# Performance work log

Measured on AMD Instinct MI355X. Metric: run time of the kernel, lower is better.

The kernel has to match this reference:

```python
import jax, jax.numpy as jnp
import numpy as np

T = 32            # num_tsteps
B = 8192          # batch_size
W_IN0, W_OUT0 = 36, 18
W_IN1, W_OUT1 = 18, 8
TILE0, TILE1 = 2, 1
BETA = (0.95, 0.95)
TH = (0.55, 0.25)
Q = 15000.0       # sephia mrr_Q
ER_DB = 20.0      # sephia extinction ratio
IL_DB = 0.0       # sephia insertion loss
SHIFT_PM = -250.0 # sephia resonance shift per unit spike
P_UNITY = 1e-4    # dbm_to_watt(-10): optical power per WDM channel at unit input


def _lif(inp, mem, beta, th):
    # snntorch Leaky, reset_mechanism='zero', reset_delay=True:
    # reset decided from incoming mem, membrane zeroed before leak+integrate.
    reset = (mem > th).astype(inp.dtype)
    mem_new = (beta * mem + inp) * (1.0 - reset)
    spk = (mem_new > th).astype(inp.dtype)
    return spk, mem_new


def _allpass(spk, wl_nm):
    # All-pass MRR modulator: spike shifts the ring resonance by SHIFT_PM.
    # Normalized detuning delta = shift / (FWHM/2), FWHM = lambda / Q.
    fwhm_pm = wl_nm * 1e3 / Q                      # [C]
    delta = (spk * SHIFT_PM) / (0.5 * fwhm_pm)     # [B, C]
    gamma = 10.0 ** (-ER_DB / 20.0)                # on-resonance amplitude (ER)
    il = 10.0 ** (-IL_DB / 20.0)                   # insertion loss factor
    return (il * (1j * delta + gamma) / (1j * delta + 1.0)).astype(jnp.complex64)


def setup_inputs() -> dict:
    key = jax.random.key(0)
    ks = jax.random.split(key, 6)
    return {
        "x_in": jax.random.uniform(ks[0], (T, B, W_IN0), jnp.float32),
        "W0": jax.random.uniform(ks[1], (TILE0, W_IN0 // TILE0, W_OUT0 * 2 // TILE0), jnp.float32),
        "d0": jax.random.normal(ks[2], (TILE0, W_OUT0 // TILE0), jnp.float32) * 5e3,
        "W1": jax.random.uniform(ks[3], (TILE1, W_IN1 // TILE1, W_OUT1 * 2 // TILE1), jnp.float32),
        "d1": jax.random.normal(ks[4], (TILE1, W_OUT1 // TILE1), jnp.float32) * 5e3,
        "peak_powers_dbm": jax.random.uniform(ks[5], (W_IN0,), jnp.float32, -15.0, -5.0),
    }


def reference(x_in, W0, d0, W1, d1, peak_powers_dbm):
    wl0 = 1550.0 + 0.8 * jnp.arange(W_OUT0, dtype=jnp.float32)   # MRR resonance wavelengths (nm)
    # sephia_inputs: sqrt(dbm_to_watt(P_dbm) * 1e6) field amplitude per channel
    amp0 = jnp.sqrt((10.0 ** (peak_powers_dbm[:W_OUT0] / 10.0) / 1000.0) * 1e6)
    S0 = W_OUT0 * 2 // TILE0   # 18 spatial channels after EO broadcast
    S1 = W_OUT1 * 2 // TILE1   # 16 spatial channels into layer 1

    def step(carry, x_t):
        mem0, mem1 = carry
        b = x_t.shape[0]
        # --- EO conversion + layer 0 MRR weight bank (power domain) ---
        p_in = x_t * P_UNITY                                     # [B, 36] optical power
        p0 = jnp.broadcast_to(p_in[:, :, None], (b, W_IN0, S0)).reshape(b, TILE0, W_IN0 // TILE0, S0)
        I0 = jnp.einsum('btws,tws->bts', p0, W0)                 # photocurrents [B,2,18]
        cur0 = ((I0[..., 0::2] - I0[..., 1::2]) * d0).reshape(b, W_OUT0)  # balanced PDs + Diagonal
        spk0, mem0 = _lif(cur0, mem0, BETA[0], TH[0])
        # --- SEPhIA all-pass MRR modulation of comb lines ---
        lo = _allpass(spk0, wl0) * amp0.astype(jnp.complex64)    # [B, 18] complex field
        pw0 = jnp.abs(lo) ** 2                                   # detected power == spike record
        # --- post-SEPhIA broadcast + layer 1 weight bank ---
        p1 = jnp.broadcast_to(pw0[:, :, None], (b, W_IN1, S1)).reshape(b, TILE1, W_IN1 // TILE1, S1)
        I1 = jnp.einsum('btws,tws->bts', p1, W1)                 # [B,1,16]
        cur1 = ((I1[..., 0::2] - I1[..., 1::2]) * d1).reshape(b, W_OUT1)
        spk1, mem1 = _lif(cur1, mem1, BETA[1], TH[1])
        return (mem0, mem1), (pw0, spk1, mem0, mem1)

    mem0 = jnp.zeros((x_in.shape[1], W_OUT0), x_in.dtype)
    mem1 = jnp.zeros((x_in.shape[1], W_OUT1), x_in.dtype)
    _, (spks0, spks1, mems0, mems1) = jax.lax.scan(step, (mem0, mem1), x_in)
    return spks0, spks1, mems0, mems1
```

## Files before the change

kernel.cpp:

```cpp
#include <hip/hip_runtime.h>


namespace {
constexpr int Tn = 32;
constexpr int Bn = 8192;
constexpr int O_PW = 0;
constexpr int O_S1 = Tn * Bn * 18;
constexpr int O_M0 = O_S1 + Tn * Bn * 8;
constexpr int O_M1 = O_M0 + Tn * Bn * 18;
}

__global__ __launch_bounds__(256, 4)
void oesnn_kernel(const float* __restrict__ x_in,
                  const float* __restrict__ W0g,
                  const float* __restrict__ d0g,
                  const float* __restrict__ W1g,
                  const float* __restrict__ d1g,
                  const float* __restrict__ peakg,
                  float* __restrict__ out)
{
    const int tid = blockIdx.x * 256 + threadIdx.x;
    const int b   = tid >> 5;
    const int g   = tid & 31;
    const int eb  = threadIdx.x >> 5;
    const bool isL0 = (g < 18);
    const bool isL1 = (g >= 18) && (g < 26);

    __shared__ float pwsh[8][20];

    float wA[18], wB[18];
    float dd = 0.f, pon = 0.f, poff = 0.f;
    int tl = 0;

    if (isL0) {
        tl = g / 9;
        const int jc = g % 9;
        dd = d0g[tl * 9 + jc];
        #pragma unroll
        for (int w = 0; w < 18; ++w) {
            const float2 p = *(const float2*)(W0g + ((tl * 18 + w) * 18 + 2 * jc));
            wA[w] = p.x;
            wB[w] = p.y;
        }
        const int c = g;
        const float wl    = 1550.0f + 0.8f * (float)c;
        const float halfw = 0.5f * (wl * 1e3f / 15000.0f);
        const float amp   = sqrtf((exp10f(peakg[c] / 10.0f) / 1000.0f) * 1e6f);
        {
            const float lr = 0.1f * amp;
            const float a  = sqrtf(lr * lr);
            poff = a * a;
        }
        {
            const float delta = -250.0f / halfw;
            const float den = fmaf(delta, delta, 1.0f);
            const float qr  = fmaf(delta, delta, 0.1f) / den;
            const float qi  = (delta - 0.1f * delta) / den;
            const float lr = qr * amp, li = qi * amp;
            const float a  = sqrtf(fmaf(lr, lr, li * li));
            pon = a * a;
        }
    } else {
        const int o = (g < 26) ? (g - 18) : 7;
        dd = d1g[o];
        #pragma unroll
        for (int w = 0; w < 18; ++w) {
            const float2 p = *(const float2*)(W1g + w * 16 + 2 * o);
            wA[w] = p.x;
            wB[w] = p.y;
        }
    }

    float mem0 = 0.f;
    float mem1 = 0.f;

    const float* xp = x_in + (size_t)b * 36 + tl * 18;
    float* opw = out + O_PW + (size_t)b * 18 + g;
    float* om0 = out + O_M0 + (size_t)b * 18 + g;
    const int o1 = isL1 ? (g - 18) : 0;
    float* os1 = out + O_S1 + (size_t)b * 8 + o1;
    float* om1 = out + O_M1 + (size_t)b * 8 + o1;

    float2 xv[9];
    if (isL0) {
        #pragma unroll
        for (int k = 0; k < 9; ++k) xv[k] = *(const float2*)(xp + 2 * k);
    }

    #pragma unroll 1
    for (int t = 0; t < Tn; ++t) {
        if (isL0) {
            float p[18];
            #pragma unroll
            for (int k = 0; k < 9; ++k) {
                p[2 * k]     = xv[k].x * 1e-4f;
                p[2 * k + 1] = xv[k].y * 1e-4f;
            }
            xp += Bn * 36;
            if (t < Tn - 1) {
                #pragma unroll
                for (int k = 0; k < 9; ++k) xv[k] = *(const float2*)(xp + 2 * k);
            }
            float se = 0.f, so = 0.f;
            #pragma unroll
            for (int w = 0; w < 18; ++w) {
                se = fmaf(p[w], wA[w], se);
                so = fmaf(p[w], wB[w], so);
            }
            const float c0 = (se - so) * dd;
            const float m2 = (mem0 > 0.55f) ? 0.0f : fmaf(0.95f, mem0, c0);
            mem0 = m2;
            const float pw = (m2 > 0.55f) ? pon : poff;

            *opw = pw;
            *om0 = m2;
            pwsh[eb][g] = pw;
        }

        if (isL1) {
            const float4 qa = *(const float4*)&pwsh[eb][0];
            const float4 qb = *(const float4*)&pwsh[eb][4];
            const float4 qc = *(const float4*)&pwsh[eb][8];
            const float4 qd = *(const float4*)&pwsh[eb][12];
            const float2 qe = *(const float2*)&pwsh[eb][16];
            const float pwall[18] = {qa.x, qa.y, qa.z, qa.w,
                                     qb.x, qb.y, qb.z, qb.w,
                                     qc.x, qc.y, qc.z, qc.w,
                                     qd.x, qd.y, qd.z, qd.w,
                                     qe.x, qe.y};
            float i1e = 0.f, i1o = 0.f;
            #pragma unroll
            for (int c = 0; c < 18; ++c) {
                i1e = fmaf(pwall[c], wA[c], i1e);
                i1o = fmaf(pwall[c], wB[c], i1o);
            }
            const float c1 = (i1e - i1o) * dd;
            const float m3 = (mem1 > 0.25f) ? 0.0f : fmaf(0.95f, mem1, c1);
            mem1 = m3;
            *os1 = (m3 > 0.25f) ? 1.0f : 0.0f;
            *om1 = m3;
        }

        opw += Bn * 18;
        om0 += Bn * 18;
        os1 += Bn * 8;
        om1 += Bn * 8;
    }
}

extern "C" void kernel_launch(void* const* d_in, const int* in_sizes, int n_in,
                              void* d_out, int out_size, void* d_ws, size_t ws_size,
                              hipStream_t stream) {
    (void)in_sizes; (void)n_in; (void)out_size; (void)d_ws; (void)ws_size;
    const float* x  = (const float*)d_in[0];
    const float* W0 = (const float*)d_in[1];
    const float* d0 = (const float*)d_in[2];
    const float* W1 = (const float*)d_in[3];
    const float* d1 = (const float*)d_in[4];
    const float* pk = (const float*)d_in[5];
    float* out = (float*)d_out;

    dim3 grid(Bn * 32 / 256), block(256);
    hipLaunchKernelGGL(oesnn_kernel, grid, block, 0, stream,
                       x, W0, d0, W1, d1, pk, out);
}
```

Baseline: 137.9 us.

## Software-pipeline layer1 one step behind layer0 with double-buffered shared spikes

Restructures the time loop to process two timesteps per iteration. Layer-1 work for step t runs interleaved with layer-0 work for step t+1, using double-buffered LDS slots, so that the two layers' latencies can overlap. The x inputs are now prefetched two steps ahead into two register buffers by all lanes, including non-L0 lanes. In exchange, register pressure rises and the idle lanes issue redundant loads. Correctness depends on the 64-wide wavefront executing in lockstep, since there are no barriers between the LDS write and read.

```diff
diff --git a/kernel.cpp b/kernel.cpp
--- a/kernel.cpp
+++ b/kernel.cpp
@@ -22,18 +22,18 @@
     const int tid = blockIdx.x * 256 + threadIdx.x;
     const int b   = tid >> 5;
     const int g   = tid & 31;
-    const int eb  = threadIdx.x >> 5;
+    const int wv  = threadIdx.x >> 6;
+    const int eh  = (threadIdx.x >> 5) & 1;
     const bool isL0 = (g < 18);
     const bool isL1 = (g >= 18) && (g < 26);
 
-    __shared__ float pwsh[8][20];
+    __shared__ float pwsh[4][2][2][20];
 
     float wA[18], wB[18];
     float dd = 0.f, pon = 0.f, poff = 0.f;
-    int tl = 0;
+    const int tl = isL0 ? (g / 9) : 0;
 
     if (isL0) {
-        tl = g / 9;
         const int jc = g % 9;
         dd = d0g[tl * 9 + jc];
         #pragma unroll
@@ -74,55 +74,28 @@
     float mem0 = 0.f;
     float mem1 = 0.f;
 
-    const float* xp = x_in + (size_t)b * 36 + tl * 18;
+    const float* xb = x_in + (size_t)b * 36 + tl * 18;
     float* opw = out + O_PW + (size_t)b * 18 + g;
     float* om0 = out + O_M0 + (size_t)b * 18 + g;
     const int o1 = isL1 ? (g - 18) : 0;
     float* os1 = out + O_S1 + (size_t)b * 8 + o1;
     float* om1 = out + O_M1 + (size_t)b * 8 + o1;
 
-    float2 xv[9];
-    if (isL0) {
+    float2 xvA[9], xvB[9];
+    {
+        const float2* s0 = (const float2*)(xb);
+        const float2* s1 = (const float2*)(xb + (size_t)Bn * 36);
         #pragma unroll
-        for (int k = 0; k < 9; ++k) xv[k] = *(const float2*)(xp + 2 * k);
+        for (int k = 0; k < 9; ++k) { xvA[k] = s0[k]; xvB[k] = s1[k]; }
     }
 
-    #pragma unroll 1
-    for (int t = 0; t < Tn; ++t) {
-        if (isL0) {
-            float p[18];
-            #pragma unroll
-            for (int k = 0; k < 9; ++k) {
-                p[2 * k]     = xv[k].x * 1e-4f;
-                p[2 * k + 1] = xv[k].y * 1e-4f;
-            }
-            xp += Bn * 36;
-            if (t < Tn - 1) {
-                #pragma unroll
-                for (int k = 0; k < 9; ++k) xv[k] = *(const float2*)(xp + 2 * k);
-            }
-            float se = 0.f, so = 0.f;
-            #pragma unroll
-            for (int w = 0; w < 18; ++w) {
-                se = fmaf(p[w], wA[w], se);
-                so = fmaf(p[w], wB[w], so);
-            }
-            const float c0 = (se - so) * dd;
-            const float m2 = (mem0 > 0.55f) ? 0.0f : fmaf(0.95f, mem0, c0);
-            mem0 = m2;
-            const float pw = (m2 > 0.55f) ? pon : poff;
-
-            *opw = pw;
-            *om0 = m2;
-            pwsh[eb][g] = pw;
-        }
-
+    auto l1phase = [&](int parr, float* os1p, float* om1p) {
         if (isL1) {
-            const float4 qa = *(const float4*)&pwsh[eb][0];
-            const float4 qb = *(const float4*)&pwsh[eb][4];
-            const float4 qc = *(const float4*)&pwsh[eb][8];
-            const float4 qd = *(const float4*)&pwsh[eb][12];
-            const float2 qe = *(const float2*)&pwsh[eb][16];
+            const float4 qa = *(const float4*)&pwsh[wv][parr][eh][0];
+            const float4 qb = *(const float4*)&pwsh[wv][parr][eh][4];
+            const float4 qc = *(const float4*)&pwsh[wv][parr][eh][8];
+            const float4 qd = *(const float4*)&pwsh[wv][parr][eh][12];
+            const float2 qe = *(const float2*)&pwsh[wv][parr][eh][16];
             const float pwall[18] = {qa.x, qa.y, qa.z, qa.w,
                                      qb.x, qb.y, qb.z, qb.w,
                                      qc.x, qc.y, qc.z, qc.w,
@@ -137,15 +110,54 @@
             const float c1 = (i1e - i1o) * dd;
             const float m3 = (mem1 > 0.25f) ? 0.0f : fmaf(0.95f, mem1, c1);
             mem1 = m3;
-            *os1 = (m3 > 0.25f) ? 1.0f : 0.0f;
-            *om1 = m3;
+            *os1p = (m3 > 0.25f) ? 1.0f : 0.0f;
+            *om1p = m3;
         }
+    };
 
-        opw += Bn * 18;
-        om0 += Bn * 18;
-        os1 += Bn * 8;
-        om1 += Bn * 8;
+    auto l0phase = [&](float2 (&xv)[9], int t, int parw,
+                       float* opwp, float* om0p) {
+        float p[18];
+        #pragma unroll
+        for (int k = 0; k < 9; ++k) {
+            p[2 * k]     = xv[k].x * 1e-4f;
+            p[2 * k + 1] = xv[k].y * 1e-4f;
+        }
+        if (t + 2 < Tn) {
+            const float2* s = (const float2*)(xb + (size_t)(t + 2) * Bn * 36);
+            #pragma unroll
+            for (int k = 0; k < 9; ++k) xv[k] = s[k];
+        }
+        if (isL0) {
+            float se = 0.f, so = 0.f;
+            #pragma unroll
+            for (int w = 0; w < 18; ++w) {
+                se = fmaf(p[w], wA[w], se);
+                so = fmaf(p[w], wB[w], so);
+            }
+            const float c0 = (se - so) * dd;
+            const float m2 = (mem0 > 0.55f) ? 0.0f : fmaf(0.95f, mem0, c0);
+            mem0 = m2;
+            const float pw = (m2 > 0.55f) ? pon : poff;
+            *opwp = pw;
+            *om0p = m2;
+            pwsh[wv][parw][eh][g] = pw;
+        }
+    };
+
+    #pragma unroll 1
+    for (int t2 = 0; t2 < Tn; t2 += 2) {
+        if (t2 > 0) l1phase(1, os1 - Bn * 8, om1 - Bn * 8);
+        l0phase(xvA, t2, 0, opw, om0);
+        l1phase(0, os1, om1);
+        l0phase(xvB, t2 + 1, 1, opw + (size_t)Bn * 18, om0 + (size_t)Bn * 18);
+
+        opw += 2 * (size_t)Bn * 18;
+        om0 += 2 * (size_t)Bn * 18;
+        os1 += 2 * (size_t)Bn * 8;
+        om1 += 2 * (size_t)Bn * 8;
     }
+    l1phase(1, os1 - Bn * 8, om1 - Bn * 8);
 }
 
 extern "C" void kernel_launch(void* const* d_in, const int* in_sizes, int n_in,
```

Result: faster. 129.3 us (-6.3%).
